# Kernel tuning notes

Measured on AMD Instinct MI355X. Metric: run time of the kernel, lower is better.

Reference implementation:

```python
import jax, jax.numpy as jnp
from jax import lax
import numpy as np

B, T = 2, 4096
NQ, NAUX, NR, NS, K = 256, 28, 512, 256, 2
DIL = [2 ** i for i in range(10)] * 3  # 30 residual blocks
L = len(DIL)


def _causal_conv(x, w, b, d):
    # x: (B, Cin, T), w: (Cout, Cin, K) -- left-pad (K-1)*d for causality
    pad = (w.shape[-1] - 1) * d
    y = lax.conv_general_dilated(x, w, window_strides=(1,), padding=[(pad, 0)],
                                 rhs_dilation=(d,),
                                 dimension_numbers=('NCH', 'OIH', 'NCH'))
    return y + b[None, :, None]


def _conv1x1(x, w, b):
    # x: (B, Cin, T), w: (Cout, Cin)
    return jnp.einsum('oc,bct->bot', w, x) + b[None, :, None]


def setup_inputs() -> dict:
    key = jax.random.key(0)
    ks = jax.random.split(key, 32)
    s = 0.05
    n = lambda k, shp: (jax.random.normal(k, shp, dtype=jnp.float32) * s)
    return {
        'x': jax.random.randint(ks[0], (B, T), 0, NQ, dtype=jnp.int32),
        'h': jax.random.normal(ks[1], (B, NAUX, T), dtype=jnp.float32),
        'causal_w': n(ks[2], (NR, NQ, K)), 'causal_b': n(ks[3], (NR,)),
        'dil_sig_w': n(ks[4], (L, NR, NR, K)), 'dil_sig_b': n(ks[5], (L, NR)),
        'dil_tanh_w': n(ks[6], (L, NR, NR, K)), 'dil_tanh_b': n(ks[7], (L, NR)),
        'aux_sig_w': n(ks[8], (L, NR, NAUX)), 'aux_sig_b': n(ks[9], (L, NR)),
        'aux_tanh_w': n(ks[10], (L, NR, NAUX)), 'aux_tanh_b': n(ks[11], (L, NR)),
        'skip_w': n(ks[12], (L, NS, NR)), 'skip_b': n(ks[13], (L, NS)),
        'res_w': n(ks[14], (L, NR, NR)), 'res_b': n(ks[15], (L, NR)),
        'post1_w': n(ks[16], (NS, NS)), 'post1_b': n(ks[17], (NS,)),
        'post2_w': n(ks[18], (NQ, NS)), 'post2_b': n(ks[19], (NQ,)),
        'lin_w': n(ks[20], (NQ, NQ)), 'lin_b': n(ks[21], (NQ,)),
    }


def reference(x, h, causal_w, causal_b, dil_sig_w, dil_sig_b, dil_tanh_w,
              dil_tanh_b, aux_sig_w, aux_sig_b, aux_tanh_w, aux_tanh_b,
              skip_w, skip_b, res_w, res_b, post1_w, post1_b, post2_w,
              post2_b, lin_w, lin_b):
    # preprocess: one-hot -> (B, NQ, T) -> causal conv
    oh = jax.nn.one_hot(x % NQ, NQ, dtype=jnp.float32).transpose(0, 2, 1)
    out = _causal_conv(oh, causal_w, causal_b, 1)  # (B, NR, T)
    skip_sum = jnp.zeros((B, NS, T), dtype=jnp.float32)
    for l, d in enumerate(DIL):
        s = _causal_conv(out, dil_sig_w[l], dil_sig_b[l], d) \
            + _conv1x1(h, aux_sig_w[l], aux_sig_b[l])
        t = _causal_conv(out, dil_tanh_w[l], dil_tanh_b[l], d) \
            + _conv1x1(h, aux_tanh_w[l], aux_tanh_b[l])
        g = jax.nn.sigmoid(s) * jnp.tanh(t)  # gated activation (B, NR, T)
        skip_sum = skip_sum + _conv1x1(g, skip_w[l], skip_b[l])
        out = _conv1x1(g, res_w[l], res_b[l]) + out  # residual
    o = jax.nn.relu(skip_sum)
    o = jax.nn.relu(_conv1x1(o, post1_w, post1_b))
    o = _conv1x1(o, post2_w, post2_b).transpose(0, 2, 1)  # (B, T, NQ)
    return o @ lin_w.T + lin_b
```

## Files before the change

kernel.cpp:

```cpp
#include <hip/hip_runtime.h>
#include <cstddef>

#define B_ 2
#define T_ 4096
#define NQ_ 256
#define NAUX_ 28
#define NR_ 512
#define NS_ 256
#define L_ 30

typedef _Float16 half_t;
typedef __attribute__((ext_vector_type(8))) _Float16 f16x8;
typedef __attribute__((ext_vector_type(4))) _Float16 f16x4;
typedef __attribute__((ext_vector_type(2))) _Float16 f16x2;
typedef __attribute__((ext_vector_type(4))) float f32x4;

__device__ inline half_t f2h(float f) { return (half_t)f; }
__device__ inline float h2f(half_t h) { return (float)h; }

__device__ __forceinline__ void gload16(const void* g, void* l) {
    __builtin_amdgcn_global_load_lds(
        (const __attribute__((address_space(1))) unsigned int*)g,
        (__attribute__((address_space(3))) unsigned int*)l, 16, 0, 0);
}

__device__ __forceinline__ void phase_barrier() {
    asm volatile("" ::: "memory");
    __builtin_amdgcn_s_barrier();
    asm volatile("" ::: "memory");
}
__device__ __forceinline__ void gate_barrier() {
    asm volatile("s_waitcnt vmcnt(6)" ::: "memory");
    __builtin_amdgcn_s_barrier();
    asm volatile("" ::: "memory");
}


__global__ __launch_bounds__(512, 2) void gates8(
    const half_t* __restrict__ actB, const half_t* __restrict__ Wf,
    const float* __restrict__ biasG, half_t* __restrict__ g,
    const half_t* __restrict__ zbuf, int dil)
{
    __shared__ __align__(16) half_t sA[3][16 * 512];
    __shared__ __align__(16) half_t sB[3][256 * 64];

    const int tid = threadIdx.x;
    const int hw = blockIdx.x + 16 * (blockIdx.y + 8 * blockIdx.z);
    const int xcd = hw & 7;
    const int jj = hw >> 3;
    const int yv = jj & 7;
    const int tBz = xcd + 8 * ((jj >> 3) & 3);
    const int b = tBz >> 4;
    const int tB = (tBz & 15) * 256;
    const int w = tid >> 6, lane = tid & 63;
    const int wm = w >> 2, wn = w & 3;
    const int l15 = lane & 15, lg = lane >> 4;
    const int rr = lane >> 3, cc = lane & 7;
    const int sc8 = cc ^ rr;
    const int mgB = yv * 8;

    f32x4 acc[4][4] = {};
    f16x8 af[4][2];

    auto stageA = [&](int v, int buf) {
#pragma unroll
        for (int s2 = 0; s2 < 2; s2++)
            gload16(&Wf[((size_t)(mgB + w) * 34 + v * 2 + s2) * 512 + lane * 8],
                    &sA[buf][(w * 2 + s2) * 512]);
    };
    auto stageB = [&](int v, int buf) {
#pragma unroll
        for (int it = 0; it < 4; it++) {
            const int t = tB + w * 32 + it * 8 + rr;
            const half_t* p;
            if (v < 8) {
                p = actB + ((size_t)b * T_ + t) * 576 + v * 64;
            } else if (v < 16) {
                const int tp = t - dil;
                p = (tp >= 0) ? actB + ((size_t)b * T_ + tp) * 576 + (v - 8) * 64
                              : zbuf;
            } else {
                p = actB + ((size_t)b * T_ + t) * 576 + 512;
            }
            gload16(p + sc8 * 8, &sB[buf][(w * 32 + it * 8) * 64]);
        }
    };
    auto loadAfrag = [&](int buf) {
#pragma unroll
        for (int i = 0; i < 4; i++)
#pragma unroll
            for (int s = 0; s < 2; s++)
                af[i][s] = *(const f16x8*)&sA[buf][((wm * 4 + i) * 2 + s) * 512 + lane * 8];
    };
    auto loadBfrag = [&](f16x8* bv, int s, int buf) {
#pragma unroll
        for (int j = 0; j < 4; j++) {
            const int r = wn * 64 + j * 16 + l15;
            bv[j] = *(const f16x8*)&sB[buf][r * 64 + (((s * 4 + lg) ^ (l15 & 7)) * 8)];
        }
    };
    auto mfma16 = [&](const f16x8* bv, int s) {
        __builtin_amdgcn_s_setprio(1);
#pragma unroll
        for (int i = 0; i < 4; i++)
#pragma unroll
            for (int j = 0; j < 4; j++)
                acc[i][j] = __builtin_amdgcn_mfma_f32_16x16x32_f16(af[i][s], bv[j], acc[i][j], 0, 0, 0);
        __builtin_amdgcn_s_setprio(0);
    };

    stageA(0, 0); stageB(0, 0);
    stageA(1, 1); stageB(1, 1);
    asm volatile("s_waitcnt vmcnt(6)" ::: "memory");
    __builtin_amdgcn_s_barrier();
    asm volatile("" ::: "memory");

    int buf = 0, nbuf = 2;
    for (int t = 0; t < 17; t++) {
        loadAfrag(buf);
        f16x8 bv0[4];
        loadBfrag(bv0, 0, buf);
        if (t + 2 < 17) stageA(t + 2, nbuf);
        phase_barrier();
        mfma16(bv0, 0);
        f16x8 bv1[4];
        loadBfrag(bv1, 1, buf);
        if (t + 2 < 17) stageB(t + 2, nbuf);
        gate_barrier();
        mfma16(bv1, 1);
        buf = (buf == 2) ? 0 : buf + 1;
        nbuf = (nbuf == 2) ? 0 : nbuf + 1;
    }

    const int gidx = yv * 2 + wm;
    const int t0 = tB + wn * 64 + l15;
#pragma unroll
    for (int i = 0; i < 2; i++) {
        const int c = gidx * 32 + i * 16 + lg * 4;
        const float4 bs = *(const float4*)&biasG[gidx * 64 + i * 16 + lg * 4];
        const float4 bt4 = *(const float4*)&biasG[gidx * 64 + 32 + i * 16 + lg * 4];
        const float bsa[4] = {bs.x, bs.y, bs.z, bs.w};
        const float bta[4] = {bt4.x, bt4.y, bt4.z, bt4.w};
#pragma unroll
        for (int j = 0; j < 4; j++) {
            const int t = t0 + j * 16;
            f16x4 o;
#pragma unroll
            for (int e = 0; e < 4; e++) {
                const float sv = acc[i][j][e] + bsa[e];
                const float tv = acc[i + 2][j][e] + bta[e];
                const float sg = 1.f / (1.f + __expf(-sv));
                const float ex = __expf(-2.f * tv);
                const float th = (1.f - ex) / (1.f + ex);
                o[e] = f2h(sg * th);
            }
            *(f16x4*)(g + ((size_t)b * T_ + t) * 512 + c) = o;
        }
    }
}

__global__ __launch_bounds__(512, 2) void res8(
    const half_t* __restrict__ X, const half_t* __restrict__ Wf,
    const float* __restrict__ bias, half_t* __restrict__ actB,
    half_t* __restrict__ skipH)
{
    __shared__ __align__(16) half_t sA[3][16 * 512];
    __shared__ __align__(16) half_t sB[3][256 * 64];

    const int tid = threadIdx.x;
    const int hw = blockIdx.x + 16 * (blockIdx.y + 6 * blockIdx.z);
    const int xcd = hw & 7;
    const int jj = hw >> 3;
    const int yv = jj % 6;
    const int tBz = xcd + 8 * (jj / 6);
    const int b = tBz >> 4;
    const int tB = (tBz & 15) * 256;
    const int mB = yv * 128;
    const int w = tid >> 6, lane = tid & 63;
    const int wm = w >> 2, wn = w & 3;
    const int l15 = lane & 15, lg = lane >> 4;
    const int rr = lane >> 3, cc = lane & 7;
    const int sc8 = cc ^ rr;
    const int mgB = yv * 8;

    f32x4 acc[4][4] = {};
    f16x8 af[4][2];

    const half_t* Xb = X + ((size_t)b * T_ + tB) * 512;

    auto stageA = [&](int v, int buf) {
#pragma unroll
        for (int s2 = 0; s2 < 2; s2++)
            gload16(&Wf[((size_t)(mgB + w) * 16 + v * 2 + s2) * 512 + lane * 8],
                    &sA[buf][(w * 2 + s2) * 512]);
    };
    auto stageB = [&](int v, int buf) {
#pragma unroll
        for (int it = 0; it < 4; it++) {
            const int row = w * 32 + it * 8;
            gload16(Xb + (size_t)(row + rr) * 512 + v * 64 + sc8 * 8,
                    &sB[buf][row * 64]);
        }
    };
    auto loadAfrag = [&](int buf) {
#pragma unroll
        for (int i = 0; i < 4; i++)
#pragma unroll
            for (int s = 0; s < 2; s++)
                af[i][s] = *(const f16x8*)&sA[buf][((wm * 4 + i) * 2 + s) * 512 + lane * 8];
    };
    auto loadBfrag = [&](f16x8* bv, int s, int buf) {
#pragma unroll
        for (int j = 0; j < 4; j++) {
            const int r = wn * 64 + j * 16 + l15;
            bv[j] = *(const f16x8*)&sB[buf][r * 64 + (((s * 4 + lg) ^ (l15 & 7)) * 8)];
        }
    };
    auto mfma16 = [&](const f16x8* bv, int s) {
        __builtin_amdgcn_s_setprio(1);
#pragma unroll
        for (int i = 0; i < 4; i++)
#pragma unroll
            for (int j = 0; j < 4; j++)
                acc[i][j] = __builtin_amdgcn_mfma_f32_16x16x32_f16(af[i][s], bv[j], acc[i][j], 0, 0, 0);
        __builtin_amdgcn_s_setprio(0);
    };

    stageA(0, 0); stageB(0, 0);
    stageA(1, 1); stageB(1, 1);
    asm volatile("s_waitcnt vmcnt(6)" ::: "memory");
    __builtin_amdgcn_s_barrier();
    asm volatile("" ::: "memory");

    int buf = 0, nbuf = 2;
    for (int t = 0; t < 8; t++) {
        loadAfrag(buf);
        f16x8 bv0[4];
        loadBfrag(bv0, 0, buf);
        if (t + 2 < 8) stageA(t + 2, nbuf);
        phase_barrier();
        mfma16(bv0, 0);
        f16x8 bv1[4];
        loadBfrag(bv1, 1, buf);
        if (t + 2 < 8) stageB(t + 2, nbuf);
        gate_barrier();
        mfma16(bv1, 1);
        buf = (buf == 2) ? 0 : buf + 1;
        nbuf = (nbuf == 2) ? 0 : nbuf + 1;
    }

    const int n0 = tB + wn * 64 + l15;
#pragma unroll
    for (int i = 0; i < 4; i++) {
        const int m = mB + wm * 64 + i * 16 + lg * 4;
        const float4 bv = *(const float4*)&bias[m];
#pragma unroll
        for (int j = 0; j < 4; j++) {
            const int t = n0 + j * 16;
            const float o0 = acc[i][j][0] + bv.x, o1 = acc[i][j][1] + bv.y;
            const float o2 = acc[i][j][2] + bv.z, o3 = acc[i][j][3] + bv.w;
            const size_t bt = (size_t)b * T_ + t;
            half_t* p = (mB + wm * 64 + i * 16 < 512)
                            ? (actB + bt * 576 + m)
                            : (skipH + bt * 256 + (m - 512));
            f16x4 old = *(const f16x4*)p;
            f16x4 nv = {f2h(h2f(old.x) + o0), f2h(h2f(old.y) + o1),
                        f2h(h2f(old.z) + o2), f2h(h2f(old.w) + o3)};
            *(f16x4*)p = nv;
        }
    }
}

template<int K, int EPI>
__global__ __launch_bounds__(256, 2) void gemm_mfma(
    const half_t* __restrict__ X, const half_t* __restrict__ Wf,
    const float* __restrict__ bias, void* __restrict__ out, int M,
    half_t* __restrict__ actB, half_t* __restrict__ skipH)
{
    constexpr int NITER = K / 128;
    constexpr int NKS = K / 32;
    __shared__ __align__(16) half_t sB[2][256 * 64];

    const int tid = threadIdx.x;
    const int b = blockIdx.z;
    const int tB = blockIdx.x * 128;
    const int mB = blockIdx.y * 128;
    const int w = tid >> 6, lane = tid & 63;
    const int wm = w >> 1, wn = w & 1;
    const int l15 = lane & 15, lg = lane >> 4;
    const int rr = lane >> 3, cc = lane & 7;
    const int sc8 = cc ^ rr;

    f32x4 acc[4][4] = {};
    f16x8 aC[8], aP[8];

    const int mgW = (mB >> 4) + wm * 4;
    const half_t* Xb = X + ((size_t)b * T_ + tB) * K;

    auto loadA = [&](f16x8* d, int v) {
#pragma unroll
        for (int i = 0; i < 4; i++)
#pragma unroll
            for (int s = 0; s < 2; s++)
                d[i * 2 + s] = *(const f16x8*)&Wf[((size_t)(mgW + i) * NKS + v * 2 + s) * 512 + lane * 8];
    };
    auto stageSlice = [&](int v, int rowbase, int buf) {
#pragma unroll
        for (int it = 0; it < 4; it++) {
            const int row = w * 32 + it * 8;
            gload16(Xb + (size_t)(row + rr) * K + v * 64 + sc8 * 8,
                    &sB[buf][(rowbase + row) * 64]);
        }
    };
    auto compute = [&](const f16x8* a, int rowbase, int buf) {
#pragma unroll
        for (int s = 0; s < 2; s++) {
            f16x8 bv[4];
#pragma unroll
            for (int j = 0; j < 4; j++) {
                const int r = rowbase + wn * 64 + j * 16 + l15;
                bv[j] = *(const f16x8*)&sB[buf][r * 64 + (((s * 4 + lg) ^ (l15 & 7)) * 8)];
            }
#pragma unroll
            for (int i = 0; i < 4; i++)
#pragma unroll
                for (int j = 0; j < 4; j++)
                    acc[i][j] = __builtin_amdgcn_mfma_f32_16x16x32_f16(a[i * 2 + s], bv[j], acc[i][j], 0, 0, 0);
        }
    };

    stageSlice(0, 0, 0);
    stageSlice(1, 128, 0);
    loadA(aC, 0);
    loadA(aP, 1);
#pragma unroll
    for (int kc = 0; kc < NITER; kc++) {
        __syncthreads();
        if (kc + 1 < NITER) {
            stageSlice(2 * kc + 2, 0, (kc + 1) & 1);
            stageSlice(2 * kc + 3, 128, (kc + 1) & 1);
        }
        compute(aC, 0, kc & 1);
        if (kc + 1 < NITER) loadA(aC, 2 * kc + 2);
        compute(aP, 128, kc & 1);
        if (kc + 1 < NITER) loadA(aP, 2 * kc + 3);
    }

    const int n0 = tB + wn * 64 + l15;
#pragma unroll
    for (int i = 0; i < 4; i++) {
        const int m = mB + wm * 64 + i * 16 + lg * 4;
        float4 bv = make_float4(0.f, 0.f, 0.f, 0.f);
        if (bias) bv = *(const float4*)&bias[m];
#pragma unroll
        for (int j = 0; j < 4; j++) {
            const int t = n0 + j * 16;
            float o0 = acc[i][j][0] + bv.x, o1 = acc[i][j][1] + bv.y;
            float o2 = acc[i][j][2] + bv.z, o3 = acc[i][j][3] + bv.w;
            if (EPI == 1) {
                o0 = fmaxf(o0, 0.f); o1 = fmaxf(o1, 0.f);
                o2 = fmaxf(o2, 0.f); o3 = fmaxf(o3, 0.f);
            }
            if (EPI == 3) {
                const size_t bt = (size_t)b * T_ + t;
                half_t* p = (mB < 512) ? (actB + bt * 576 + m)
                                       : (skipH + bt * 256 + (m - 512));
                f16x4 old = *(const f16x4*)p;
                f16x4 nv = {f2h(h2f(old.x) + o0), f2h(h2f(old.y) + o1),
                            f2h(h2f(old.z) + o2), f2h(h2f(old.w) + o3)};
                *(f16x4*)p = nv;
            } else {
                const size_t off = ((size_t)b * T_ + t) * M + m;
                if (EPI == 2) {
                    *(float4*)((float*)out + off) = make_float4(o0, o1, o2, o3);
                } else {
                    f16x4 ov = {f2h(o0), f2h(o1), f2h(o2), f2h(o3)};
                    *(f16x4*)((half_t*)out + off) = ov;
                }
            }
        }
    }
}

__global__ __launch_bounds__(256) void relupack_kernel(
    const half_t* __restrict__ skipH, half_t* __restrict__ outp)
{
    const int idx = blockIdx.x * 256 + threadIdx.x;
    const int c = (idx & 63) * 4;
    const int bt = idx >> 6;
    const f16x4 v = *(const f16x4*)(skipH + (size_t)bt * 256 + c);
    f16x4 o = {f2h(fmaxf(h2f(v.x), 0.f)), f2h(fmaxf(h2f(v.y), 0.f)),
               f2h(fmaxf(h2f(v.z), 0.f)), f2h(fmaxf(h2f(v.w), 0.f))};
    *(f16x4*)(outp + (size_t)bt * 256 + c) = o;
}

__global__ __launch_bounds__(256) void embed_kernel(
    const int* __restrict__ x, const float* __restrict__ cw,
    const float* __restrict__ cb, half_t* __restrict__ actB)
{
    const int t = blockIdx.x, b = blockIdx.y;
    const int idc = x[b * T_ + t];
    const int idp = (t > 0) ? x[b * T_ + t - 1] : -1;
    const size_t bt = (size_t)b * T_ + t;
    for (int c = threadIdx.x; c < 512; c += 256) {
        float v = cw[(c * 256 + idc) * 2 + 1] + cb[c];
        if (idp >= 0) v += cw[(c * 256 + idp) * 2 + 0];
        actB[bt * 576 + c] = f2h(v);
    }
}

__global__ __launch_bounds__(256) void packh_kernel(
    const float* __restrict__ h, half_t* __restrict__ actB)
{
    const int idx = blockIdx.x * 256 + threadIdx.x;
    const int j = idx & 63;
    const int bt = idx >> 6;
    const int b = bt >> 12, t = bt & 4095;
    const float v = (j < 28) ? h[((size_t)b * NAUX_ + j) * T_ + t] : 0.f;
    actB[(size_t)bt * 576 + 512 + j] = f2h(v);
}

__global__ __launch_bounds__(256) void packgate_kernel(
    const float* __restrict__ dsw, const float* __restrict__ dtw,
    half_t* __restrict__ Wg)
{
    __shared__ half_t lds[16 * 1040];
    const int mg = blockIdx.x;
    const int l  = blockIdx.y;
    const int tid = threadIdx.x;
    const int rsub0 = (mg * 16) & 63;
    const int c0 = ((mg * 16) >> 6) * 32 + (rsub0 & 31);
    const float* src = ((rsub0 < 32) ? dsw : dtw) + ((size_t)(l * 512 + c0)) * 1024;
    const int row = tid >> 4, gq = tid & 15;
    const float4* srow = (const float4*)(src + (size_t)row * 1024);
#pragma unroll
    for (int u = 0; u < 16; u++) {
        const int q = u * 16 + gq;
        const float4 v = srow[q];
        *(f16x2*)&lds[row * 1040 + 2 * q]       = f16x2{f2h(v.x), f2h(v.z)};
        *(f16x2*)&lds[row * 1040 + 512 + 2 * q] = f16x2{f2h(v.y), f2h(v.w)};
    }
    __syncthreads();
    const int lane = tid & 63, wv = tid >> 6;
    half_t* dst = Wg + (size_t)l * 1114112 + (size_t)mg * 34 * 512;
#pragma unroll
    for (int v = 0; v < 8; v++) {
        const int s = wv + 4 * v;
        const int tap = (s < 16) ? 1 : 0;
        const f16x8 val = *(const f16x8*)&lds[(lane & 15) * 1040 + tap * 512
                                              + (s & 15) * 32 + (lane >> 4) * 8];
        *(f16x8*)&dst[((size_t)s * 64 + lane) * 8] = val;
    }
}

__global__ __launch_bounds__(256) void packgaux_kernel(
    const float* __restrict__ asw, const float* __restrict__ atw,
    half_t* __restrict__ Wg)
{
    const int idx = blockIdx.x * 256 + threadIdx.x;
    const int lane = idx & 63;
    const int ksd = (idx >> 6) & 1;
    const int mg = (idx >> 7) & 63;
    const int l = idx >> 13;
    const int r = mg * 16 + (lane & 15);
    const int rsub = r & 63;
    const int c = (r >> 6) * 32 + (rsub & 31);
    const float* src = (rsub < 32) ? asw : atw;
    const int j0 = ksd * 32 + (lane >> 4) * 8;
    f16x8 v = {};
#pragma unroll
    for (int e = 0; e < 8; e++) {
        const int j = j0 + e;
        if (j < NAUX_) v[e] = f2h(src[(size_t)(l * 512 + c) * NAUX_ + j]);
    }
    Wg += (size_t)l * 1114112;
    *(f16x8*)&Wg[((size_t)(mg * 34 + 32 + ksd) * 64 + lane) * 8] = v;
}

__global__ __launch_bounds__(256) void packsr_kernel(
    const float* __restrict__ rsw, const float* __restrict__ skw,
    half_t* __restrict__ Wsr)
{
    __shared__ half_t lds[16 * 520];
    const int mg = blockIdx.x;
    const int l  = blockIdx.y;
    const int tid = threadIdx.x;
    const int r0 = mg * 16;
    const float* src = (r0 < 512) ? (rsw + ((size_t)l * 512 + r0) * 512)
                                  : (skw + ((size_t)l * 256 + (r0 - 512)) * 512);
    const int row = tid >> 4, gq = tid & 15;
    const float4* srow = (const float4*)(src + (size_t)row * 512);
#pragma unroll
    for (int u = 0; u < 8; u++) {
        const int q = u * 16 + gq;
        const float4 v = srow[q];
        f16x4 h4 = {f2h(v.x), f2h(v.y), f2h(v.z), f2h(v.w)};
        *(f16x4*)&lds[row * 520 + 4 * q] = h4;
    }
    __syncthreads();
    const int lane = tid & 63, wv = tid >> 6;
    half_t* dst = Wsr + (size_t)l * 393216 + (size_t)mg * 16 * 512;
#pragma unroll
    for (int v = 0; v < 4; v++) {
        const int s = wv + 4 * v;
        const f16x8 val = *(const f16x8*)&lds[(lane & 15) * 520 + s * 32 + (lane >> 4) * 8];
        *(f16x8*)&dst[((size_t)s * 64 + lane) * 8] = val;
    }
}

__global__ __launch_bounds__(256) void packpost_kernel(
    const float* __restrict__ p1w, const float* __restrict__ p2w,
    const float* __restrict__ lw, half_t* __restrict__ Wpost)
{
    const int idx = blockIdx.x * 256 + threadIdx.x;
    const int lane = idx & 63;
    const int ks = (idx >> 6) & 7;
    const int mg = (idx >> 9) & 15;
    const int mi = idx >> 13;
    const float* src = (mi == 0) ? p1w : (mi == 1) ? p2w : lw;
    const int r = mg * 16 + (lane & 15);
    const int kb = ks * 32 + (lane >> 4) * 8;
    const float4 q0 = ((const float4*)(src + (size_t)r * 256 + kb))[0];
    const float4 q1 = ((const float4*)(src + (size_t)r * 256 + kb))[1];
    f16x8 v = {f2h(q0.x), f2h(q0.y), f2h(q0.z), f2h(q0.w),
               f2h(q1.x), f2h(q1.y), f2h(q1.z), f2h(q1.w)};
    *(f16x8*)&Wpost[(size_t)mi * 65536 + ((size_t)(mg * 8 + ks) * 64 + lane) * 8] = v;
}

__global__ __launch_bounds__(256) void packbias_kernel(
    const float* __restrict__ dsb, const float* __restrict__ asb,
    const float* __restrict__ dtb, const float* __restrict__ atb,
    const float* __restrict__ rsb, const float* __restrict__ skb,
    float* __restrict__ biasG, float* __restrict__ biasSr)
{
    const int idx = blockIdx.x * 256 + threadIdx.x;
    if (idx < 30 * 1024) {
        const int l = idx >> 10, r = idx & 1023;
        const int rsub = r & 63;
        const int c = (r >> 6) * 32 + (rsub & 31);
        const float v = (rsub < 32) ? (dsb[l * 512 + c] + asb[l * 512 + c])
                                    : (dtb[l * 512 + c] + atb[l * 512 + c]);
        biasG[idx] = v;
    } else if (idx < 30 * 1024 + 30 * 768) {
        const int j = idx - 30 * 1024;
        const int l = j / 768, r = j % 768;
        biasSr[j] = (r < 512) ? rsb[l * 512 + r] : skb[l * 256 + (r - 512)];
    }
}

extern "C" void kernel_launch(void* const* d_in, const int* in_sizes, int n_in,
                              void* d_out, int out_size, void* d_ws, size_t ws_size,
                              hipStream_t stream)
{
    (void)in_sizes; (void)n_in; (void)out_size; (void)ws_size;

    const int* x = (const int*)d_in[0];
    const float* h = (const float*)d_in[1];
    const float* causal_w = (const float*)d_in[2];
    const float* causal_b = (const float*)d_in[3];
    const float* dsw = (const float*)d_in[4];
    const float* dsb = (const float*)d_in[5];
    const float* dtw = (const float*)d_in[6];
    const float* dtb = (const float*)d_in[7];
    const float* asw = (const float*)d_in[8];
    const float* asb = (const float*)d_in[9];
    const float* atw = (const float*)d_in[10];
    const float* atb = (const float*)d_in[11];
    const float* skw = (const float*)d_in[12];
    const float* skb = (const float*)d_in[13];
    const float* rsw = (const float*)d_in[14];
    const float* rsb = (const float*)d_in[15];
    const float* p1w = (const float*)d_in[16];
    const float* p1b = (const float*)d_in[17];
    const float* p2w = (const float*)d_in[18];
    const float* p2b = (const float*)d_in[19];
    const float* lw  = (const float*)d_in[20];
    const float* lb  = (const float*)d_in[21];

    char* ws = (char*)d_ws;
    size_t off = 0;
    auto alloc = [&](size_t bytes) { char* p = ws + off; off += (bytes + 255) & ~(size_t)255; return p; };

    half_t* Wg     = (half_t*)alloc((size_t)L_ * 1114112 * 2);
    half_t* Wsr    = (half_t*)alloc((size_t)L_ * 393216 * 2);
    half_t* Wpost  = (half_t*)alloc((size_t)3 * 65536 * 2);
    float*  biasG  = (float*) alloc((size_t)L_ * 1024 * 4);
    float*  biasSr = (float*) alloc((size_t)L_ * 768 * 4);
    half_t* actB   = (half_t*)alloc((size_t)B_ * T_ * 576 * 2);
    half_t* g      = (half_t*)alloc((size_t)B_ * T_ * 512 * 2);
    half_t* skipH  = (half_t*)alloc((size_t)B_ * T_ * 256 * 2);
    half_t* zbuf   = (half_t*)alloc(256);
    half_t* pA     = (half_t*)alloc((size_t)B_ * T_ * 256 * 2);
    half_t* pB     = (half_t*)alloc((size_t)B_ * T_ * 256 * 2);

    hipMemsetAsync(skipH, 0, (size_t)B_ * T_ * 256 * 2 + 256, stream);

    packgate_kernel<<<dim3(64, 30), 256, 0, stream>>>(dsw, dtw, Wg);
    packgaux_kernel<<<30 * 64 * 2 * 64 / 256, 256, 0, stream>>>(asw, atw, Wg);
    packsr_kernel<<<dim3(48, 30), 256, 0, stream>>>(rsw, skw, Wsr);
    packpost_kernel<<<3 * 16 * 8 * 64 / 256, 256, 0, stream>>>(p1w, p2w, lw, Wpost);
    packbias_kernel<<<(30 * 1024 + 30 * 768 + 255) / 256, 256, 0, stream>>>(
        dsb, asb, dtb, atb, rsb, skb, biasG, biasSr);
    packh_kernel<<<B_ * T_ * 64 / 256, 256, 0, stream>>>(h, actB);
    embed_kernel<<<dim3(T_, B_), 256, 0, stream>>>(x, causal_w, causal_b, actB);

    for (int l = 0; l < L_; l++) {
        const int dil = 1 << (l % 10);
        gates8<<<dim3(16, 8, B_), 512, 0, stream>>>(
            actB, Wg + (size_t)l * 1114112, biasG + (size_t)l * 1024, g, zbuf, dil);
        res8<<<dim3(16, 6, B_), 512, 0, stream>>>(
            g, Wsr + (size_t)l * 393216, biasSr + (size_t)l * 768, actB, skipH);
    }

    relupack_kernel<<<B_ * T_ * 64 / 256, 256, 0, stream>>>(skipH, pA);
    gemm_mfma<256, 1><<<dim3(32, 2, B_), 256, 0, stream>>>(pA, Wpost, p1b, pB, 256,
                                                           nullptr, nullptr);
    gemm_mfma<256, 0><<<dim3(32, 2, B_), 256, 0, stream>>>(pB, Wpost + 65536, p2b, pA, 256,
                                                           nullptr, nullptr);
    gemm_mfma<256, 2><<<dim3(32, 2, B_), 256, 0, stream>>>(pA, Wpost + 131072, lb, d_out, 256,
                                                           nullptr, nullptr);
}
```

Before: 1.513 ms.

## Fuse gate and residual/skip GEMMs into one per-layer kernel with flag sync

Merges the per-layer gates and residual/skip kernels into a single launch. Each block computes its gate tile, publishes completion through an atomic per-time-tile counter, then spins until all 8 channel-group blocks for that time tile have written g before running the residual/skip GEMM. The activation buffer is double-buffered (ping-pong actB0/actB1) so the residual update does not race with other blocks still reading the layer input. This halves launch count and removes a kernel boundary per layer, but relies on all 256 blocks being co-resident for the spin-wait, and the residual phase leaves two of eight waves idle when staging weights.

```diff
diff --git a/kernel.cpp b/kernel.cpp
--- a/kernel.cpp
+++ b/kernel.cpp
@@ -29,69 +29,31 @@
     __builtin_amdgcn_s_barrier();
     asm volatile("" ::: "memory");
 }
-__device__ __forceinline__ void gate_barrier() {
-    asm volatile("s_waitcnt vmcnt(6)" ::: "memory");
-    __builtin_amdgcn_s_barrier();
-    asm volatile("" ::: "memory");
-}
-
-
-__global__ __launch_bounds__(512, 2) void gates8(
-    const half_t* __restrict__ actB, const half_t* __restrict__ Wf,
-    const float* __restrict__ biasG, half_t* __restrict__ g,
-    const half_t* __restrict__ zbuf, int dil)
+
+
+__global__ __launch_bounds__(512, 2) void layer_fused(
+    const half_t* __restrict__ actB_in, half_t* __restrict__ actB_out,
+    const half_t* __restrict__ Wg_l, const float* __restrict__ biasG,
+    half_t* __restrict__ g, const half_t* __restrict__ Wsr_l,
+    const float* __restrict__ biasSr, half_t* __restrict__ skipH,
+    const half_t* __restrict__ zbuf, int* __restrict__ flag, int dil)
 {
     __shared__ __align__(16) half_t sA[3][16 * 512];
     __shared__ __align__(16) half_t sB[3][256 * 64];
 
     const int tid = threadIdx.x;
-    const int hw = blockIdx.x + 16 * (blockIdx.y + 8 * blockIdx.z);
-    const int xcd = hw & 7;
-    const int jj = hw >> 3;
-    const int yv = jj & 7;
-    const int tBz = xcd + 8 * ((jj >> 3) & 3);
-    const int b = tBz >> 4;
-    const int tB = (tBz & 15) * 256;
+    const int tBi = blockIdx.x;
+    const int yv  = blockIdx.y;
+    const int b   = blockIdx.z;
+    const int tB  = tBi * 256;
     const int w = tid >> 6, lane = tid & 63;
     const int wm = w >> 2, wn = w & 3;
     const int l15 = lane & 15, lg = lane >> 4;
     const int rr = lane >> 3, cc = lane & 7;
     const int sc8 = cc ^ rr;
-    const int mgB = yv * 8;
-
-    f32x4 acc[4][4] = {};
+
     f16x8 af[4][2];
 
-    auto stageA = [&](int v, int buf) {
-#pragma unroll
-        for (int s2 = 0; s2 < 2; s2++)
-            gload16(&Wf[((size_t)(mgB + w) * 34 + v * 2 + s2) * 512 + lane * 8],
-                    &sA[buf][(w * 2 + s2) * 512]);
-    };
-    auto stageB = [&](int v, int buf) {
-#pragma unroll
-        for (int it = 0; it < 4; it++) {
-            const int t = tB + w * 32 + it * 8 + rr;
-            const half_t* p;
-            if (v < 8) {
-                p = actB + ((size_t)b * T_ + t) * 576 + v * 64;
-            } else if (v < 16) {
-                const int tp = t - dil;
-                p = (tp >= 0) ? actB + ((size_t)b * T_ + tp) * 576 + (v - 8) * 64
-                              : zbuf;
-            } else {
-                p = actB + ((size_t)b * T_ + t) * 576 + 512;
-            }
-            gload16(p + sc8 * 8, &sB[buf][(w * 32 + it * 8) * 64]);
-        }
-    };
-    auto loadAfrag = [&](int buf) {
-#pragma unroll
-        for (int i = 0; i < 4; i++)
-#pragma unroll
-            for (int s = 0; s < 2; s++)
-                af[i][s] = *(const f16x8*)&sA[buf][((wm * 4 + i) * 2 + s) * 512 + lane * 8];
-    };
     auto loadBfrag = [&](f16x8* bv, int s, int buf) {
 #pragma unroll
         for (int j = 0; j < 4; j++) {
@@ -99,174 +61,221 @@
             bv[j] = *(const f16x8*)&sB[buf][r * 64 + (((s * 4 + lg) ^ (l15 & 7)) * 8)];
         }
     };
-    auto mfma16 = [&](const f16x8* bv, int s) {
-        __builtin_amdgcn_s_setprio(1);
-#pragma unroll
-        for (int i = 0; i < 4; i++)
-#pragma unroll
-            for (int j = 0; j < 4; j++)
-                acc[i][j] = __builtin_amdgcn_mfma_f32_16x16x32_f16(af[i][s], bv[j], acc[i][j], 0, 0, 0);
-        __builtin_amdgcn_s_setprio(0);
-    };
-
-    stageA(0, 0); stageB(0, 0);
-    stageA(1, 1); stageB(1, 1);
-    asm volatile("s_waitcnt vmcnt(6)" ::: "memory");
-    __builtin_amdgcn_s_barrier();
-    asm volatile("" ::: "memory");
-
-    int buf = 0, nbuf = 2;
-    for (int t = 0; t < 17; t++) {
-        loadAfrag(buf);
-        f16x8 bv0[4];
-        loadBfrag(bv0, 0, buf);
-        if (t + 2 < 17) stageA(t + 2, nbuf);
-        phase_barrier();
-        mfma16(bv0, 0);
-        f16x8 bv1[4];
-        loadBfrag(bv1, 1, buf);
-        if (t + 2 < 17) stageB(t + 2, nbuf);
-        gate_barrier();
-        mfma16(bv1, 1);
-        buf = (buf == 2) ? 0 : buf + 1;
-        nbuf = (nbuf == 2) ? 0 : nbuf + 1;
-    }
-
-    const int gidx = yv * 2 + wm;
-    const int t0 = tB + wn * 64 + l15;
-#pragma unroll
-    for (int i = 0; i < 2; i++) {
-        const int c = gidx * 32 + i * 16 + lg * 4;
-        const float4 bs = *(const float4*)&biasG[gidx * 64 + i * 16 + lg * 4];
-        const float4 bt4 = *(const float4*)&biasG[gidx * 64 + 32 + i * 16 + lg * 4];
-        const float bsa[4] = {bs.x, bs.y, bs.z, bs.w};
-        const float bta[4] = {bt4.x, bt4.y, bt4.z, bt4.w};
-#pragma unroll
-        for (int j = 0; j < 4; j++) {
-            const int t = t0 + j * 16;
-            f16x4 o;
-#pragma unroll
-            for (int e = 0; e < 4; e++) {
-                const float sv = acc[i][j][e] + bsa[e];
-                const float tv = acc[i + 2][j][e] + bta[e];
-                const float sg = 1.f / (1.f + __expf(-sv));
-                const float ex = __expf(-2.f * tv);
-                const float th = (1.f - ex) / (1.f + ex);
-                o[e] = f2h(sg * th);
-            }
-            *(f16x4*)(g + ((size_t)b * T_ + t) * 512 + c) = o;
-        }
-    }
-}
-
-__global__ __launch_bounds__(512, 2) void res8(
-    const half_t* __restrict__ X, const half_t* __restrict__ Wf,
-    const float* __restrict__ bias, half_t* __restrict__ actB,
-    half_t* __restrict__ skipH)
-{
-    __shared__ __align__(16) half_t sA[3][16 * 512];
-    __shared__ __align__(16) half_t sB[3][256 * 64];
-
-    const int tid = threadIdx.x;
-    const int hw = blockIdx.x + 16 * (blockIdx.y + 6 * blockIdx.z);
-    const int xcd = hw & 7;
-    const int jj = hw >> 3;
-    const int yv = jj % 6;
-    const int tBz = xcd + 8 * (jj / 6);
-    const int b = tBz >> 4;
-    const int tB = (tBz & 15) * 256;
-    const int mB = yv * 128;
-    const int w = tid >> 6, lane = tid & 63;
-    const int wm = w >> 2, wn = w & 3;
-    const int l15 = lane & 15, lg = lane >> 4;
-    const int rr = lane >> 3, cc = lane & 7;
-    const int sc8 = cc ^ rr;
-    const int mgB = yv * 8;
-
-    f32x4 acc[4][4] = {};
-    f16x8 af[4][2];
-
-    const half_t* Xb = X + ((size_t)b * T_ + tB) * 512;
-
-    auto stageA = [&](int v, int buf) {
-#pragma unroll
-        for (int s2 = 0; s2 < 2; s2++)
-            gload16(&Wf[((size_t)(mgB + w) * 16 + v * 2 + s2) * 512 + lane * 8],
-                    &sA[buf][(w * 2 + s2) * 512]);
-    };
-    auto stageB = [&](int v, int buf) {
-#pragma unroll
-        for (int it = 0; it < 4; it++) {
-            const int row = w * 32 + it * 8;
-            gload16(Xb + (size_t)(row + rr) * 512 + v * 64 + sc8 * 8,
-                    &sB[buf][row * 64]);
-        }
-    };
-    auto loadAfrag = [&](int buf) {
-#pragma unroll
-        for (int i = 0; i < 4; i++)
-#pragma unroll
-            for (int s = 0; s < 2; s++)
-                af[i][s] = *(const f16x8*)&sA[buf][((wm * 4 + i) * 2 + s) * 512 + lane * 8];
-    };
-    auto loadBfrag = [&](f16x8* bv, int s, int buf) {
-#pragma unroll
-        for (int j = 0; j < 4; j++) {
-            const int r = wn * 64 + j * 16 + l15;
-            bv[j] = *(const f16x8*)&sB[buf][r * 64 + (((s * 4 + lg) ^ (l15 & 7)) * 8)];
-        }
-    };
-    auto mfma16 = [&](const f16x8* bv, int s) {
-        __builtin_amdgcn_s_setprio(1);
-#pragma unroll
-        for (int i = 0; i < 4; i++)
-#pragma unroll
-            for (int j = 0; j < 4; j++)
-                acc[i][j] = __builtin_amdgcn_mfma_f32_16x16x32_f16(af[i][s], bv[j], acc[i][j], 0, 0, 0);
-        __builtin_amdgcn_s_setprio(0);
-    };
-
-    stageA(0, 0); stageB(0, 0);
-    stageA(1, 1); stageB(1, 1);
-    asm volatile("s_waitcnt vmcnt(6)" ::: "memory");
-    __builtin_amdgcn_s_barrier();
-    asm volatile("" ::: "memory");
-
-    int buf = 0, nbuf = 2;
-    for (int t = 0; t < 8; t++) {
-        loadAfrag(buf);
-        f16x8 bv0[4];
-        loadBfrag(bv0, 0, buf);
-        if (t + 2 < 8) stageA(t + 2, nbuf);
-        phase_barrier();
-        mfma16(bv0, 0);
-        f16x8 bv1[4];
-        loadBfrag(bv1, 1, buf);
-        if (t + 2 < 8) stageB(t + 2, nbuf);
-        gate_barrier();
-        mfma16(bv1, 1);
-        buf = (buf == 2) ? 0 : buf + 1;
-        nbuf = (nbuf == 2) ? 0 : nbuf + 1;
-    }
-
-    const int n0 = tB + wn * 64 + l15;
-#pragma unroll
-    for (int i = 0; i < 4; i++) {
-        const int m = mB + wm * 64 + i * 16 + lg * 4;
-        const float4 bv = *(const float4*)&bias[m];
-#pragma unroll
-        for (int j = 0; j < 4; j++) {
-            const int t = n0 + j * 16;
-            const float o0 = acc[i][j][0] + bv.x, o1 = acc[i][j][1] + bv.y;
-            const float o2 = acc[i][j][2] + bv.z, o3 = acc[i][j][3] + bv.w;
-            const size_t bt = (size_t)b * T_ + t;
-            half_t* p = (mB + wm * 64 + i * 16 < 512)
-                            ? (actB + bt * 576 + m)
-                            : (skipH + bt * 256 + (m - 512));
-            f16x4 old = *(const f16x4*)p;
-            f16x4 nv = {f2h(h2f(old.x) + o0), f2h(h2f(old.y) + o1),
-                        f2h(h2f(old.z) + o2), f2h(h2f(old.w) + o3)};
-            *(f16x4*)p = nv;
+
+    {
+        const int mgB = yv * 8;
+        f32x4 acc[4][4] = {};
+
+        auto stageA = [&](int v, int buf) {
+#pragma unroll
+            for (int s2 = 0; s2 < 2; s2++)
+                gload16(&Wg_l[((size_t)(mgB + w) * 34 + v * 2 + s2) * 512 + lane * 8],
+                        &sA[buf][(w * 2 + s2) * 512]);
+        };
+        auto stageB = [&](int v, int buf) {
+#pragma unroll
+            for (int it = 0; it < 4; it++) {
+                const int t = tB + w * 32 + it * 8 + rr;
+                const half_t* p;
+                if (v < 8) {
+                    p = actB_in + ((size_t)b * T_ + t) * 576 + v * 64;
+                } else if (v < 16) {
+                    const int tp = t - dil;
+                    p = (tp >= 0) ? actB_in + ((size_t)b * T_ + tp) * 576 + (v - 8) * 64
+                                  : zbuf;
+                } else {
+                    p = actB_in + ((size_t)b * T_ + t) * 576 + 512;
+                }
+                gload16(p + sc8 * 8, &sB[buf][(w * 32 + it * 8) * 64]);
+            }
+        };
+        auto loadAfrag = [&](int buf) {
+#pragma unroll
+            for (int i = 0; i < 4; i++)
+#pragma unroll
+                for (int s = 0; s < 2; s++)
+                    af[i][s] = *(const f16x8*)&sA[buf][((wm * 4 + i) * 2 + s) * 512 + lane * 8];
+        };
+        auto mfma16 = [&](const f16x8* bv, int s) {
+            __builtin_amdgcn_s_setprio(1);
+#pragma unroll
+            for (int i = 0; i < 4; i++)
+#pragma unroll
+                for (int j = 0; j < 4; j++)
+                    acc[i][j] = __builtin_amdgcn_mfma_f32_16x16x32_f16(af[i][s], bv[j], acc[i][j], 0, 0, 0);
+            __builtin_amdgcn_s_setprio(0);
+        };
+
+        stageA(0, 0); stageB(0, 0);
+        stageA(1, 1); stageB(1, 1);
+        asm volatile("s_waitcnt vmcnt(6)" ::: "memory");
+        __builtin_amdgcn_s_barrier();
+        asm volatile("" ::: "memory");
+
+        int buf = 0, nbuf = 2;
+        for (int kt = 0; kt < 17; kt++) {
+            loadAfrag(buf);
+            f16x8 bv0[4];
+            loadBfrag(bv0, 0, buf);
+            if (kt + 2 < 17) stageA(kt + 2, nbuf);
+            phase_barrier();
+            mfma16(bv0, 0);
+            f16x8 bv1[4];
+            loadBfrag(bv1, 1, buf);
+            if (kt + 2 < 17) {
+                stageB(kt + 2, nbuf);
+                asm volatile("s_waitcnt vmcnt(6)" ::: "memory");
+            } else {
+                asm volatile("s_waitcnt vmcnt(0)" ::: "memory");
+            }
+            __builtin_amdgcn_s_barrier();
+            asm volatile("" ::: "memory");
+            mfma16(bv1, 1);
+            buf = (buf == 2) ? 0 : buf + 1;
+            nbuf = (nbuf == 2) ? 0 : nbuf + 1;
+        }
+
+        const int gidx = yv * 2 + wm;
+        const int t0 = tB + wn * 64 + l15;
+#pragma unroll
+        for (int i = 0; i < 2; i++) {
+            const int c = gidx * 32 + i * 16 + lg * 4;
+            const float4 bs = *(const float4*)&biasG[gidx * 64 + i * 16 + lg * 4];
+            const float4 bt4 = *(const float4*)&biasG[gidx * 64 + 32 + i * 16 + lg * 4];
+            const float bsa[4] = {bs.x, bs.y, bs.z, bs.w};
+            const float bta[4] = {bt4.x, bt4.y, bt4.z, bt4.w};
+#pragma unroll
+            for (int j = 0; j < 4; j++) {
+                const int t = t0 + j * 16;
+                f16x4 o;
+#pragma unroll
+                for (int e = 0; e < 4; e++) {
+                    const float sv = acc[i][j][e] + bsa[e];
+                    const float tv = acc[i + 2][j][e] + bta[e];
+                    const float sg = 1.f / (1.f + __expf(-sv));
+                    const float ex = __expf(-2.f * tv);
+                    const float th = (1.f - ex) / (1.f + ex);
+                    o[e] = f2h(sg * th);
+                }
+                *(f16x4*)(g + ((size_t)b * T_ + t) * 512 + c) = o;
+            }
+        }
+    }
+
+    __threadfence();
+    __syncthreads();
+    if (tid == 0)
+        __hip_atomic_fetch_add(&flag[b * 16 + tBi], 1,
+                               __ATOMIC_RELEASE, __HIP_MEMORY_SCOPE_AGENT);
+
+    {
+        const int mgBr = yv * 6;
+        f32x4 acc[3][4] = {};
+        const half_t* Xb = g + ((size_t)b * T_ + tB) * 512;
+
+        auto stageAr = [&](int v, int buf) {
+            if (w < 6) {
+#pragma unroll
+                for (int s2 = 0; s2 < 2; s2++)
+                    gload16(&Wsr_l[((size_t)(mgBr + w) * 16 + v * 2 + s2) * 512 + lane * 8],
+                            &sA[buf][(w * 2 + s2) * 512]);
+            }
+        };
+        auto stageBr = [&](int v, int buf) {
+#pragma unroll
+            for (int it = 0; it < 4; it++) {
+                const int row = w * 32 + it * 8;
+                gload16(Xb + (size_t)(row + rr) * 512 + v * 64 + sc8 * 8,
+                        &sB[buf][row * 64]);
+            }
+        };
+        auto loadAfragr = [&](int buf) {
+#pragma unroll
+            for (int i = 0; i < 3; i++)
+#pragma unroll
+                for (int s = 0; s < 2; s++)
+                    af[i][s] = *(const f16x8*)&sA[buf][((wm * 3 + i) * 2 + s) * 512 + lane * 8];
+        };
+        auto mfma12 = [&](const f16x8* bv, int s) {
+            __builtin_amdgcn_s_setprio(1);
+#pragma unroll
+            for (int i = 0; i < 3; i++)
+#pragma unroll
+                for (int j = 0; j < 4; j++)
+                    acc[i][j] = __builtin_amdgcn_mfma_f32_16x16x32_f16(af[i][s], bv[j], acc[i][j], 0, 0, 0);
+            __builtin_amdgcn_s_setprio(0);
+        };
+
+        stageAr(0, 0);
+        stageAr(1, 1);
+        if (tid == 0) {
+            int fv, guard = 0;
+            do {
+                fv = __hip_atomic_load(&flag[b * 16 + tBi],
+                                       __ATOMIC_ACQUIRE, __HIP_MEMORY_SCOPE_AGENT);
+                if (fv < 8) {
+                    __builtin_amdgcn_s_sleep(8);
+                    if (++guard > (1 << 20)) break;
+                }
+            } while (fv < 8);
+        }
+        __syncthreads();
+        stageBr(0, 0);
+        stageBr(1, 1);
+        asm volatile("s_waitcnt vmcnt(4)" ::: "memory");
+        __builtin_amdgcn_s_barrier();
+        asm volatile("" ::: "memory");
+
+        int buf = 0, nbuf = 2;
+        for (int kt = 0; kt < 8; kt++) {
+            loadAfragr(buf);
+            f16x8 bv0[4];
+            loadBfrag(bv0, 0, buf);
+            if (kt + 2 < 8) stageAr(kt + 2, nbuf);
+            phase_barrier();
+            mfma12(bv0, 0);
+            f16x8 bv1[4];
+            loadBfrag(bv1, 1, buf);
+            if (kt + 2 < 8) {
+                stageBr(kt + 2, nbuf);
+                if (w < 6) asm volatile("s_waitcnt vmcnt(6)" ::: "memory");
+                else       asm volatile("s_waitcnt vmcnt(4)" ::: "memory");
+            } else {
+                asm volatile("s_waitcnt vmcnt(0)" ::: "memory");
+            }
+            __builtin_amdgcn_s_barrier();
+            asm volatile("" ::: "memory");
+            mfma12(bv1, 1);
+            buf = (buf == 2) ? 0 : buf + 1;
+            nbuf = (nbuf == 2) ? 0 : nbuf + 1;
+        }
+
+        const int n0 = tB + wn * 64 + l15;
+#pragma unroll
+        for (int i = 0; i < 3; i++) {
+            const int mrow = yv * 96 + wm * 48 + i * 16;
+            const int m = mrow + lg * 4;
+            const float4 bv = *(const float4*)&biasSr[m];
+#pragma unroll
+            for (int j = 0; j < 4; j++) {
+                const int t = n0 + j * 16;
+                const float o0 = acc[i][j][0] + bv.x, o1 = acc[i][j][1] + bv.y;
+                const float o2 = acc[i][j][2] + bv.z, o3 = acc[i][j][3] + bv.w;
+                const size_t bt = (size_t)b * T_ + t;
+                half_t* p;
+                const half_t* pold;
+                if (mrow < 512) {
+                    p = actB_out + bt * 576 + m;
+                    pold = actB_in + bt * 576 + m;
+                } else {
+                    p = skipH + bt * 256 + (m - 512);
+                    pold = p;
+                }
+                f16x4 old = *(const f16x4*)pold;
+                f16x4 nv = {f2h(h2f(old.x) + o0), f2h(h2f(old.y) + o1),
+                            f2h(h2f(old.z) + o2), f2h(h2f(old.w) + o3)};
+                *(f16x4*)p = nv;
+            }
         }
     }
 }
@@ -274,8 +283,7 @@
 template<int K, int EPI>
 __global__ __launch_bounds__(256, 2) void gemm_mfma(
     const half_t* __restrict__ X, const half_t* __restrict__ Wf,
-    const float* __restrict__ bias, void* __restrict__ out, int M,
-    half_t* __restrict__ actB, half_t* __restrict__ skipH)
+    const float* __restrict__ bias, void* __restrict__ out, int M)
 {
     constexpr int NITER = K / 128;
     constexpr int NKS = K / 32;
@@ -361,22 +369,12 @@
                 o0 = fmaxf(o0, 0.f); o1 = fmaxf(o1, 0.f);
                 o2 = fmaxf(o2, 0.f); o3 = fmaxf(o3, 0.f);
             }
-            if (EPI == 3) {
-                const size_t bt = (size_t)b * T_ + t;
-                half_t* p = (mB < 512) ? (actB + bt * 576 + m)
-                                       : (skipH + bt * 256 + (m - 512));
-                f16x4 old = *(const f16x4*)p;
-                f16x4 nv = {f2h(h2f(old.x) + o0), f2h(h2f(old.y) + o1),
-                            f2h(h2f(old.z) + o2), f2h(h2f(old.w) + o3)};
-                *(f16x4*)p = nv;
+            const size_t off = ((size_t)b * T_ + t) * M + m;
+            if (EPI == 2) {
+                *(float4*)((float*)out + off) = make_float4(o0, o1, o2, o3);
             } else {
-                const size_t off = ((size_t)b * T_ + t) * M + m;
-                if (EPI == 2) {
-                    *(float4*)((float*)out + off) = make_float4(o0, o1, o2, o3);
-                } else {
-                    f16x4 ov = {f2h(o0), f2h(o1), f2h(o2), f2h(o3)};
-                    *(f16x4*)((half_t*)out + off) = ov;
-                }
+                f16x4 ov = {f2h(o0), f2h(o1), f2h(o2), f2h(o3)};
+                *(f16x4*)((half_t*)out + off) = ov;
             }
         }
     }
@@ -396,7 +394,7 @@
 
 __global__ __launch_bounds__(256) void embed_kernel(
     const int* __restrict__ x, const float* __restrict__ cw,
-    const float* __restrict__ cb, half_t* __restrict__ actB)
+    const float* __restrict__ cb, half_t* __restrict__ actB0)
 {
     const int t = blockIdx.x, b = blockIdx.y;
     const int idc = x[b * T_ + t];
@@ -405,26 +403,29 @@
     for (int c = threadIdx.x; c < 512; c += 256) {
         float v = cw[(c * 256 + idc) * 2 + 1] + cb[c];
         if (idp >= 0) v += cw[(c * 256 + idp) * 2 + 0];
-        actB[bt * 576 + c] = f2h(v);
+        actB0[bt * 576 + c] = f2h(v);
     }
 }
 
 __global__ __launch_bounds__(256) void packh_kernel(
-    const float* __restrict__ h, half_t* __restrict__ actB)
+    const float* __restrict__ h, half_t* __restrict__ actB0,
+    half_t* __restrict__ actB1)
 {
     const int idx = blockIdx.x * 256 + threadIdx.x;
     const int j = idx & 63;
     const int bt = idx >> 6;
     const int b = bt >> 12, t = bt & 4095;
     const float v = (j < 28) ? h[((size_t)b * NAUX_ + j) * T_ + t] : 0.f;
-    actB[(size_t)bt * 576 + 512 + j] = f2h(v);
+    const half_t hv = f2h(v);
+    actB0[(size_t)bt * 576 + 512 + j] = hv;
+    actB1[(size_t)bt * 576 + 512 + j] = hv;
 }
 
 __global__ __launch_bounds__(256) void packgate_kernel(
     const float* __restrict__ dsw, const float* __restrict__ dtw,
     half_t* __restrict__ Wg)
 {
-    __shared__ half_t lds[16 * 1040];
+    __shared__ half_t lds[16 * 1048];
     const int mg = blockIdx.x;
     const int l  = blockIdx.y;
     const int tid = threadIdx.x;
@@ -437,8 +438,8 @@
     for (int u = 0; u < 16; u++) {
         const int q = u * 16 + gq;
         const float4 v = srow[q];
-        *(f16x2*)&lds[row * 1040 + 2 * q]       = f16x2{f2h(v.x), f2h(v.z)};
-        *(f16x2*)&lds[row * 1040 + 512 + 2 * q] = f16x2{f2h(v.y), f2h(v.w)};
+        *(f16x2*)&lds[row * 1048 + 2 * q]       = f16x2{f2h(v.x), f2h(v.z)};
+        *(f16x2*)&lds[row * 1048 + 512 + 2 * q] = f16x2{f2h(v.y), f2h(v.w)};
     }
     __syncthreads();
     const int lane = tid & 63, wv = tid >> 6;
@@ -447,7 +448,7 @@
     for (int v = 0; v < 8; v++) {
         const int s = wv + 4 * v;
         const int tap = (s < 16) ? 1 : 0;
-        const f16x8 val = *(const f16x8*)&lds[(lane & 15) * 1040 + tap * 512
+        const f16x8 val = *(const f16x8*)&lds[(lane & 15) * 1048 + tap * 512
                                               + (s & 15) * 32 + (lane >> 4) * 8];
         *(f16x8*)&dst[((size_t)s * 64 + lane) * 8] = val;
     }
@@ -586,14 +587,16 @@
     half_t* Wpost  = (half_t*)alloc((size_t)3 * 65536 * 2);
     float*  biasG  = (float*) alloc((size_t)L_ * 1024 * 4);
     float*  biasSr = (float*) alloc((size_t)L_ * 768 * 4);
-    half_t* actB   = (half_t*)alloc((size_t)B_ * T_ * 576 * 2);
+    half_t* actB0  = (half_t*)alloc((size_t)B_ * T_ * 576 * 2);
+    half_t* actB1  = (half_t*)alloc((size_t)B_ * T_ * 576 * 2);
     half_t* g      = (half_t*)alloc((size_t)B_ * T_ * 512 * 2);
     half_t* skipH  = (half_t*)alloc((size_t)B_ * T_ * 256 * 2);
     half_t* zbuf   = (half_t*)alloc(256);
+    int*    flags  = (int*)   alloc((size_t)L_ * 32 * 4);
     half_t* pA     = (half_t*)alloc((size_t)B_ * T_ * 256 * 2);
     half_t* pB     = (half_t*)alloc((size_t)B_ * T_ * 256 * 2);
 
-    hipMemsetAsync(skipH, 0, (size_t)B_ * T_ * 256 * 2 + 256, stream);
+    hipMemsetAsync(skipH, 0, (size_t)B_ * T_ * 256 * 2 + 256 + (size_t)L_ * 32 * 4, stream);
 
     packgate_kernel<<<dim3(64, 30), 256, 0, stream>>>(dsw, dtw, Wg);
     packgaux_kernel<<<30 * 64 * 2 * 64 / 256, 256, 0, stream>>>(asw, atw, Wg);
@@ -601,22 +604,21 @@
     packpost_kernel<<<3 * 16 * 8 * 64 / 256, 256, 0, stream>>>(p1w, p2w, lw, Wpost);
     packbias_kernel<<<(30 * 1024 + 30 * 768 + 255) / 256, 256, 0, stream>>>(
         dsb, asb, dtb, atb, rsb, skb, biasG, biasSr);
-    packh_kernel<<<B_ * T_ * 64 / 256, 256, 0, stream>>>(h, actB);
-    embed_kernel<<<dim3(T_, B_), 256, 0, stream>>>(x, causal_w, causal_b, actB);
+    packh_kernel<<<B_ * T_ * 64 / 256, 256, 0, stream>>>(h, actB0, actB1);
+    embed_kernel<<<dim3(T_, B_), 256, 0, stream>>>(x, causal_w, causal_b, actB0);
 
     for (int l = 0; l < L_; l++) {
         const int dil = 1 << (l % 10);
-        gates8<<<dim3(16, 8, B_), 512, 0, stream>>>(
-            actB, Wg + (size_t)l * 1114112, biasG + (size_t)l * 1024, g, zbuf, dil);
-        res8<<<dim3(16, 6, B_), 512, 0, stream>>>(
-            g, Wsr + (size_t)l * 393216, biasSr + (size_t)l * 768, actB, skipH);
+        half_t* aIn  = (l & 1) ? actB1 : actB0;
+        half_t* aOut = (l & 1) ? actB0 : actB1;
+        layer_fused<<<dim3(16, 8, B_), 512, 0, stream>>>(
+            aIn, aOut, Wg + (size_t)l * 1114112, biasG + (size_t)l * 1024, g,
+            Wsr + (size_t)l * 393216, biasSr + (size_t)l * 768,
+            skipH, zbuf, flags + (size_t)l * 32, dil);
     }
 
     relupack_kernel<<<B_ * T_ * 64 / 256, 256, 0, stream>>>(skipH, pA);
-    gemm_mfma<256, 1><<<dim3(32, 2, B_), 256, 0, stream>>>(pA, Wpost, p1b, pB, 256,
-                                                           nullptr, nullptr);
-    gemm_mfma<256, 0><<<dim3(32, 2, B_), 256, 0, stream>>>(pB, Wpost + 65536, p2b, pA, 256,
-                                                           nullptr, nullptr);
-    gemm_mfma<256, 2><<<dim3(32, 2, B_), 256, 0, stream>>>(pA, Wpost + 131072, lb, d_out, 256,
-                                                           nullptr, nullptr);
-}
+    gemm_mfma<256, 1><<<dim3(32, 2, B_), 256, 0, stream>>>(pA, Wpost, p1b, pB, 256);
+    gemm_mfma<256, 0><<<dim3(32, 2, B_), 256, 0, stream>>>(pB, Wpost + 65536, p2b, pA, 256);
+    gemm_mfma<256, 2><<<dim3(32, 2, B_), 256, 0, stream>>>(pA, Wpost + 131072, lb, d_out, 256);
+}
```

Result: slower. 3.373 ms (+123.0%).
